# Kernel optimization log

Hardware: AMD Instinct MI355X
Metric: run time of the kernel (lower is better)

## Reference

```python
import jax, jax.numpy as jnp
import numpy as np

N_NODES = 100000
N_EDGES = 640000
D_IN = 128
D_OUT = 128


def setup_inputs() -> dict:
    key = jax.random.key(0)
    k_x, k_w, k_v, k_r, k_c = jax.random.split(key, 5)
    x = jax.random.normal(k_x, (N_NODES, D_IN), dtype=jnp.float32)
    # Xavier-uniform init for weights, zeros for bias (matches module init)
    limit = float(np.sqrt(6.0 / (D_IN + D_OUT)))
    weights = jax.random.uniform(k_w, (D_IN, D_OUT), dtype=jnp.float32,
                                 minval=-limit, maxval=limit)
    bias = jnp.zeros((D_OUT,), dtype=jnp.float32)
    # Sparse normalized adjacency in COO form: value[e] * y[col[e]] scattered to row[e]
    edge_val = jax.random.uniform(k_v, (N_EDGES,), dtype=jnp.float32)
    row = jax.random.randint(k_r, (N_EDGES,), 0, N_NODES, dtype=jnp.int32)
    col = jax.random.randint(k_c, (N_EDGES,), 0, N_NODES, dtype=jnp.int32)
    return {"x": x, "weights": weights, "bias": bias,
            "edge_val": edge_val, "row": row, "col": col}


def reference(x, weights, bias, edge_val, row, col):
    # y = x @ W  (dense GEMM)  [N, D_OUT]
    y = x @ weights
    # SpMM: out[i] = sum_{e: row[e]==i} edge_val[e] * y[col[e]]
    msg = edge_val[:, None] * y[col]            # [E, D_OUT] irregular gather
    agg = jax.ops.segment_sum(msg, row, num_segments=x.shape[0])
    return agg + bias
```

## Files before the change

### kernel.cpp

```cpp
#include <hip/hip_runtime.h>
#include <hip/hip_bf16.h>


#define N_NODES 100000
#define N_EDGES 640000
#define D 128
#define ELL_K 16
#define OVF_CAP 8192
#define NB 391
#define BCAP 2048
#define CHUNK 4096
#define NCHUNKS 157
#define N_TILES 6250
#define YT_P 132

typedef __attribute__((ext_vector_type(8))) short short8;
typedef __attribute__((ext_vector_type(4))) float f32x4;
typedef __attribute__((ext_vector_type(4))) ushort us4;

__device__ __forceinline__ ushort f2bf(float f) {
    __hip_bfloat16 h = __float2bfloat16(f);
    return __builtin_bit_cast(ushort, h);
}
__device__ __forceinline__ float bflo(uint u) { return __uint_as_float(u << 16); }
__device__ __forceinline__ float bfhi(uint u) { return __uint_as_float(u & 0xffff0000u); }

__global__ __launch_bounds__(256, 2) void gemm_xw(const float* __restrict__ x,
                                                  const float* __restrict__ w,
                                                  ushort* __restrict__ y,
                                                  int* __restrict__ bucketCnt) {
    __shared__ ushort wt[128 * 128];
    __shared__ ushort ytile[4][16 * YT_P];
    const int tid = threadIdx.x;

    int gz = blockIdx.x * 256 + tid;
    if (gz <= NB) bucketCnt[gz] = 0;

    #pragma unroll
    for (int it = 0; it < 16; ++it) {
        int idx4 = tid + it * 256;
        int k = idx4 >> 5;
        int n0 = (idx4 & 31) * 4;
        float4 v = *(const float4*)(w + (size_t)idx4 * 4);
        float vv[4] = {v.x, v.y, v.z, v.w};
        #pragma unroll
        for (int q = 0; q < 4; ++q) {
            int n = n0 + q;
            wt[n * 128 + (k ^ ((n & 7) << 3))] = f2bf(vv[q]);
        }
    }
    __syncthreads();

    const int lane = tid & 63;
    const int l15 = lane & 15;
    const int h = lane >> 4;
    const int wv = tid >> 6;
    ushort* yt = &ytile[wv][0];

    short8 bfr[8][4];
    #pragma unroll
    for (int j = 0; j < 8; ++j) {
        int n = 16 * j + l15;
        #pragma unroll
        for (int ks = 0; ks < 4; ++ks) {
            int k0 = 32 * ks + 8 * h;
            bfr[j][ks] = *(const short8*)&wt[n * 128 + (k0 ^ ((n & 7) << 3))];
        }
    }

    const int waveGlobal = blockIdx.x * 4 + wv;
    const int nWaves = gridDim.x * 4;

    int t = waveGlobal;
    if (t < N_TILES) {
        short8 a[4];
        {
            const float* xr = x + (size_t)(t * 16 + l15) * D;
            float4 xb[8];
            #pragma unroll
            for (int ks = 0; ks < 4; ++ks) {
                xb[2 * ks]     = *(const float4*)(xr + 32 * ks + 8 * h);
                xb[2 * ks + 1] = *(const float4*)(xr + 32 * ks + 8 * h + 4);
            }
            #pragma unroll
            for (int ks = 0; ks < 4; ++ks) {
                const float* p0 = (const float*)&xb[2 * ks];
                const float* p1 = (const float*)&xb[2 * ks + 1];
                a[ks][0] = f2bf(p0[0]); a[ks][1] = f2bf(p0[1]);
                a[ks][2] = f2bf(p0[2]); a[ks][3] = f2bf(p0[3]);
                a[ks][4] = f2bf(p1[0]); a[ks][5] = f2bf(p1[1]);
                a[ks][6] = f2bf(p1[2]); a[ks][7] = f2bf(p1[3]);
            }
        }
        #pragma unroll 1
        while (true) {
            const int tn = t + nWaves;
            const bool more = tn < N_TILES;

            float4 xb2[8];
            if (more) {
                const float* xr = x + (size_t)(tn * 16 + l15) * D;
                #pragma unroll
                for (int ks = 0; ks < 4; ++ks) {
                    xb2[2 * ks]     = *(const float4*)(xr + 32 * ks + 8 * h);
                    xb2[2 * ks + 1] = *(const float4*)(xr + 32 * ks + 8 * h + 4);
                }
            }

            f32x4 acc[8];
            #pragma unroll
            for (int j = 0; j < 8; ++j) acc[j] = (f32x4){0.f, 0.f, 0.f, 0.f};
            #pragma unroll
            for (int ks = 0; ks < 4; ++ks) {
                #pragma unroll
                for (int j = 0; j < 8; ++j)
                    acc[j] = __builtin_amdgcn_mfma_f32_16x16x32_bf16(bfr[j][ks], a[ks], acc[j], 0, 0, 0);
            }

            #pragma unroll
            for (int j = 0; j < 8; ++j) {
                us4 o;
                o.x = f2bf(acc[j][0]); o.y = f2bf(acc[j][1]);
                o.z = f2bf(acc[j][2]); o.w = f2bf(acc[j][3]);
                *(us4*)(yt + l15 * YT_P + 16 * j + 4 * h) = o;
            }
            ushort* yn = y + (size_t)(t * 16) * D;
            #pragma unroll
            for (int q = 0; q < 4; ++q) {
                int nl = 4 * q + h;
                float4 v = *(const float4*)(yt + nl * YT_P + l15 * 8);
                *(float4*)(yn + (size_t)nl * D + l15 * 8) = v;
            }

            if (!more) break;
            #pragma unroll
            for (int ks = 0; ks < 4; ++ks) {
                const float* p0 = (const float*)&xb2[2 * ks];
                const float* p1 = (const float*)&xb2[2 * ks + 1];
                a[ks][0] = f2bf(p0[0]); a[ks][1] = f2bf(p0[1]);
                a[ks][2] = f2bf(p0[2]); a[ks][3] = f2bf(p0[3]);
                a[ks][4] = f2bf(p1[0]); a[ks][5] = f2bf(p1[1]);
                a[ks][6] = f2bf(p1[2]); a[ks][7] = f2bf(p1[3]);
            }
            t = tn;
        }
    }
}

__global__ __launch_bounds__(256) void partition_edges(const float* __restrict__ ev,
                                                       const int* __restrict__ row,
                                                       const int* __restrict__ col,
                                                       int* __restrict__ bucketCnt,
                                                       uint2* __restrict__ es0,
                                                       int* __restrict__ ovfCnt,
                                                       int* __restrict__ ovfRow,
                                                       int* __restrict__ ovfCol,
                                                       float* __restrict__ ovfVal) {
    __shared__ int hist[NB];
    __shared__ int cur[NB];
    const int tid = threadIdx.x;
    const int base = blockIdx.x * CHUNK;

    for (int t = tid; t < NB; t += 256) hist[t] = 0;
    __syncthreads();

    #pragma unroll
    for (int it = 0; it < CHUNK / 256; ++it) {
        int i = base + it * 256 + tid;
        if (i < N_EDGES) atomicAdd(&hist[row[i] >> 8], 1);
    }
    __syncthreads();

    for (int t = tid; t < NB; t += 256) {
        int h = hist[t];
        int start = (h > 0) ? atomicAdd(&bucketCnt[t], h) : 0;
        cur[t] = t * BCAP + start;
    }
    __syncthreads();

    #pragma unroll
    for (int it = 0; it < CHUNK / 256; ++it) {
        int i = base + it * 256 + tid;
        if (i < N_EDGES) {
            int r = row[i];
            int b = r >> 8;
            int p = atomicAdd(&cur[b], 1);
            if (p < (b + 1) * BCAP) {
                uint2 e;
                e.x = __float_as_uint(ev[i]);
                e.y = (uint)col[i] | ((uint)(r & 255) << 20);
                es0[p] = e;
            } else {
                int q = atomicAdd(ovfCnt, 1);
                if (q < OVF_CAP) {
                    ovfRow[q] = r;
                    ovfCol[q] = col[i];
                    ovfVal[q] = ev[i];
                }
            }
        }
    }
}

__global__ __launch_bounds__(256) void build_ell(const uint2* __restrict__ es0,
                                                 const int* __restrict__ bucketCnt,
                                                 float2* __restrict__ es,
                                                 int* __restrict__ counts,
                                                 int* __restrict__ ovfCnt,
                                                 int* __restrict__ ovfRow,
                                                 int* __restrict__ ovfCol,
                                                 float* __restrict__ ovfVal) {
    __shared__ float2 ell[256 * ELL_K];
    __shared__ int lcnt[256];
    const int tid = threadIdx.x;
    const int b = blockIdx.x;

    lcnt[tid] = 0;
    __syncthreads();

    int cnt = bucketCnt[b];
    if (cnt > BCAP) cnt = BCAP;
    const uint2* src = es0 + (size_t)b * BCAP;

    for (int i = tid; i < cnt; i += 256) {
        uint2 e = src[i];
        int r = e.y >> 20;
        int p = atomicAdd(&lcnt[r], 1);
        if (p < ELL_K) {
            float2 rec;
            rec.x = __uint_as_float(e.x);
            rec.y = __uint_as_float(e.y & 0xFFFFFu);
            ell[r * ELL_K + p] = rec;
        } else {
            int q = atomicAdd(ovfCnt, 1);
            if (q < OVF_CAP) {
                ovfRow[q] = b * 256 + r;
                ovfCol[q] = (int)(e.y & 0xFFFFFu);
                ovfVal[q] = __uint_as_float(e.x);
            }
        }
    }
    __syncthreads();

    const int nbase = b * 256;
    int nvalid = N_NODES - nbase;
    if (nvalid > 256) nvalid = 256;

    if (tid < nvalid) counts[nbase + tid] = lcnt[tid];

    float4* dst4 = (float4*)(es + (size_t)nbase * ELL_K);
    const float4* ell4 = (const float4*)ell;
    for (int t = tid; t < nvalid * (ELL_K / 2); t += 256)
        dst4[t] = ell4[t];
}

__global__ __launch_bounds__(256) void spmm_ell(const ushort* __restrict__ y,
                                                const float2* __restrict__ es,
                                                const int* __restrict__ counts,
                                                const float* __restrict__ bias,
                                                float* __restrict__ out) {
    const int tid = threadIdx.x;
    const int lane = tid & 63;
    const int c16 = lane & 15;
    const int sub = lane >> 4;
    const int wid = blockIdx.x * 4 + (tid >> 6);

    const float4 b0 = *(const float4*)(bias + c16 * 8);
    const float4 b1 = *(const float4*)(bias + c16 * 8 + 4);

    #pragma unroll 1
    for (int rep = 0; rep < 2; ++rep) {
        const int n = wid * 8 + rep * 4 + sub;
        int deg = counts[n];
        if (deg > ELL_K) deg = ELL_K;
        const float4* er = (const float4*)(es + (size_t)n * ELL_K);

        float a0 = 0.f, a1 = 0.f, a2 = 0.f, a3 = 0.f;
        float a4 = 0.f, a5 = 0.f, a6 = 0.f, a7 = 0.f;

        #pragma unroll
        for (int g = 0; g < 4; ++g) {
            if (4 * g < deg) {
                float4 sA = er[2 * g];
                float4 sB = er[2 * g + 1];
                int c0 = __float_as_int(sA.y);
                int c1 = (4 * g + 1 < deg) ? __float_as_int(sA.w) : c0;
                int c2 = (4 * g + 2 < deg) ? __float_as_int(sB.y) : c0;
                int c3 = (4 * g + 3 < deg) ? __float_as_int(sB.w) : c0;
                uint4 u0 = *(const uint4*)(y + ((size_t)c0 << 7) + c16 * 8);
                uint4 u1 = *(const uint4*)(y + ((size_t)c1 << 7) + c16 * 8);
                uint4 u2 = *(const uint4*)(y + ((size_t)c2 << 7) + c16 * 8);
                uint4 u3 = *(const uint4*)(y + ((size_t)c3 << 7) + c16 * 8);
                float v0 = sA.x;
                float v1 = (4 * g + 1 < deg) ? sA.z : 0.f;
                float v2 = (4 * g + 2 < deg) ? sB.x : 0.f;
                float v3 = (4 * g + 3 < deg) ? sB.z : 0.f;
                a0 += v0 * bflo(u0.x); a1 += v0 * bfhi(u0.x);
                a2 += v0 * bflo(u0.y); a3 += v0 * bfhi(u0.y);
                a4 += v0 * bflo(u0.z); a5 += v0 * bfhi(u0.z);
                a6 += v0 * bflo(u0.w); a7 += v0 * bfhi(u0.w);
                a0 += v1 * bflo(u1.x); a1 += v1 * bfhi(u1.x);
                a2 += v1 * bflo(u1.y); a3 += v1 * bfhi(u1.y);
                a4 += v1 * bflo(u1.z); a5 += v1 * bfhi(u1.z);
                a6 += v1 * bflo(u1.w); a7 += v1 * bfhi(u1.w);
                a0 += v2 * bflo(u2.x); a1 += v2 * bfhi(u2.x);
                a2 += v2 * bflo(u2.y); a3 += v2 * bfhi(u2.y);
                a4 += v2 * bflo(u2.z); a5 += v2 * bfhi(u2.z);
                a6 += v2 * bflo(u2.w); a7 += v2 * bfhi(u2.w);
                a0 += v3 * bflo(u3.x); a1 += v3 * bfhi(u3.x);
                a2 += v3 * bflo(u3.y); a3 += v3 * bfhi(u3.y);
                a4 += v3 * bflo(u3.z); a5 += v3 * bfhi(u3.z);
                a6 += v3 * bflo(u3.w); a7 += v3 * bfhi(u3.w);
            }
        }
        float4 o0 = {a0 + b0.x, a1 + b0.y, a2 + b0.z, a3 + b0.w};
        float4 o1 = {a4 + b1.x, a5 + b1.y, a6 + b1.z, a7 + b1.w};
        float* orow = out + ((size_t)n << 7) + c16 * 8;
        *(float4*)orow = o0;
        *(float4*)(orow + 4) = o1;
    }
}

__global__ void ovf_fix(const ushort* __restrict__ y, const int* __restrict__ ovfRow,
                        const int* __restrict__ ovfCol, const float* __restrict__ ovfVal,
                        const int* __restrict__ ovfCnt, float* __restrict__ out) {
    int nOvf = *ovfCnt;
    if (nOvf > OVF_CAP) nOvf = OVF_CAP;
    int total = nOvf * 32;
    for (int idx = blockIdx.x * 256 + threadIdx.x; idx < total; idx += gridDim.x * 256) {
        int e = idx >> 5;
        int c = idx & 31;
        int r = ovfRow[e];
        int col = ovfCol[e];
        float v = ovfVal[e];
        uint2 u = *(const uint2*)(y + ((size_t)col << 7) + c * 4);
        atomicAdd(&out[(size_t)r * D + c * 4 + 0], v * bflo(u.x));
        atomicAdd(&out[(size_t)r * D + c * 4 + 1], v * bfhi(u.x));
        atomicAdd(&out[(size_t)r * D + c * 4 + 2], v * bflo(u.y));
        atomicAdd(&out[(size_t)r * D + c * 4 + 3], v * bfhi(u.y));
    }
}

extern "C" void kernel_launch(void* const* d_in, const int* in_sizes, int n_in,
                              void* d_out, int out_size, void* d_ws, size_t ws_size,
                              hipStream_t stream) {
    const float* x = (const float*)d_in[0];
    const float* w = (const float*)d_in[1];
    const float* bias = (const float*)d_in[2];
    const float* ev = (const float*)d_in[3];
    const int* row = (const int*)d_in[4];
    const int* col = (const int*)d_in[5];
    float* out = (float*)d_out;

    size_t off = 0;
    auto carve = [&](size_t bytes) -> void* {
        void* p = (char*)d_ws + off;
        off += (bytes + 255) & ~(size_t)255;
        return p;
    };
    ushort* y = (ushort*)carve((size_t)N_NODES * D * sizeof(ushort));
    int* counts = (int*)carve((size_t)N_NODES * sizeof(int));
    float2* es = (float2*)carve((size_t)N_NODES * ELL_K * sizeof(float2));
    uint2* es0 = (uint2*)carve((size_t)NB * BCAP * sizeof(uint2));
    int* bucketCnt = (int*)carve((NB + 1) * sizeof(int));
    int* ovfCnt = bucketCnt + NB;
    int* ovfRow = (int*)carve(OVF_CAP * sizeof(int));
    int* ovfCol = (int*)carve(OVF_CAP * sizeof(int));
    float* ovfVal = (float*)carve(OVF_CAP * sizeof(float));

    gemm_xw<<<512, 256, 0, stream>>>(x, w, y, bucketCnt);
    partition_edges<<<NCHUNKS, 256, 0, stream>>>(ev, row, col, bucketCnt, es0,
                                                 ovfCnt, ovfRow, ovfCol, ovfVal);
    build_ell<<<NB, 256, 0, stream>>>(es0, bucketCnt, es, counts,
                                      ovfCnt, ovfRow, ovfCol, ovfVal);
    spmm_ell<<<N_NODES / 32, 256, 0, stream>>>(y, es, counts, bias, out);
    ovf_fix<<<16, 256, 0, stream>>>(y, ovfRow, ovfCol, ovfVal, ovfCnt, out);
}
```

Measured before the change: 83.70 us.

## Fuse edge partitioning into GEMM kernel with atomic dynamic tile scheduling

Merges the edge-partition kernel into the GEMM kernel. The first NCHUNKS blocks bucket edges before they join the GEMM, and all waves pull 16-row tiles from a global atomic ticket counter instead of a static stride, so blocks that did partition work simply take fewer tiles. This removes one kernel launch and lets partitioning overlap with the GEMM, but adds a memset launch and a global atomic per tile. The cross-iteration x prefetch is also reduced: the next tile's load now happens after the y store rather than before the MFMAs.

```diff
diff --git a/kernel.cpp b/kernel.cpp
--- a/kernel.cpp
+++ b/kernel.cpp
@@ -13,6 +13,7 @@
 #define NCHUNKS 157
 #define N_TILES 6250
 #define YT_P 132
+#define GRID 512
 
 typedef __attribute__((ext_vector_type(8))) short short8;
 typedef __attribute__((ext_vector_type(4))) float f32x4;
@@ -25,16 +26,66 @@
 __device__ __forceinline__ float bflo(uint u) { return __uint_as_float(u << 16); }
 __device__ __forceinline__ float bfhi(uint u) { return __uint_as_float(u & 0xffff0000u); }
 
-__global__ __launch_bounds__(256, 2) void gemm_xw(const float* __restrict__ x,
-                                                  const float* __restrict__ w,
-                                                  ushort* __restrict__ y,
-                                                  int* __restrict__ bucketCnt) {
-    __shared__ ushort wt[128 * 128];
-    __shared__ ushort ytile[4][16 * YT_P];
+__global__ __launch_bounds__(256, 2) void gemm_part(const float* __restrict__ x,
+                                                    const float* __restrict__ w,
+                                                    ushort* __restrict__ y,
+                                                    const float* __restrict__ ev,
+                                                    const int* __restrict__ row,
+                                                    const int* __restrict__ col,
+                                                    uint2* __restrict__ es0,
+                                                    int* __restrict__ ctrl,
+                                                    int* __restrict__ ovfRow,
+                                                    int* __restrict__ ovfCol,
+                                                    float* __restrict__ ovfVal) {
+    __shared__ union {
+        struct { ushort wt[128 * 128]; ushort ytile[4][16 * YT_P]; } g;
+        struct { int hist[NB]; int cur[NB]; } p;
+    } sm;
     const int tid = threadIdx.x;
-
-    int gz = blockIdx.x * 256 + tid;
-    if (gz <= NB) bucketCnt[gz] = 0;
+    int* tick = ctrl + 0;
+    int* ovfCnt = ctrl + 1;
+    int* bucketCnt = ctrl + 2;
+
+    if (blockIdx.x < NCHUNKS) {
+        const int base = blockIdx.x * CHUNK;
+        for (int t = tid; t < NB; t += 256) sm.p.hist[t] = 0;
+        __syncthreads();
+        #pragma unroll
+        for (int it = 0; it < CHUNK / 256; ++it) {
+            int i = base + it * 256 + tid;
+            if (i < N_EDGES) atomicAdd(&sm.p.hist[row[i] >> 8], 1);
+        }
+        __syncthreads();
+        for (int t = tid; t < NB; t += 256) {
+            int h = sm.p.hist[t];
+            int start = (h > 0) ? atomicAdd(&bucketCnt[t], h) : 0;
+            sm.p.cur[t] = t * BCAP + start;
+        }
+        __syncthreads();
+        #pragma unroll
+        for (int it = 0; it < CHUNK / 256; ++it) {
+            int i = base + it * 256 + tid;
+            if (i < N_EDGES) {
+                int r = row[i];
+                int b = r >> 8;
+                int p = atomicAdd(&sm.p.cur[b], 1);
+                if (p < (b + 1) * BCAP) {
+                    uint2 e;
+                    e.x = __float_as_uint(ev[i]);
+                    e.y = (uint)col[i] | ((uint)(r & 255) << 20);
+                    es0[p] = e;
+                } else {
+                    int q = atomicAdd(ovfCnt, 1);
+                    if (q < OVF_CAP) {
+                        ovfRow[q] = r;
+                        ovfCol[q] = col[i];
+                        ovfVal[q] = ev[i];
+                    }
+                }
+            }
+        }
+        __syncthreads();
+    }
 
     #pragma unroll
     for (int it = 0; it < 16; ++it) {
@@ -46,7 +97,7 @@
         #pragma unroll
         for (int q = 0; q < 4; ++q) {
             int n = n0 + q;
-            wt[n * 128 + (k ^ ((n & 7) << 3))] = f2bf(vv[q]);
+            sm.g.wt[n * 128 + (k ^ ((n & 7) << 3))] = f2bf(vv[q]);
         }
     }
     __syncthreads();
@@ -55,7 +106,7 @@
     const int l15 = lane & 15;
     const int h = lane >> 4;
     const int wv = tid >> 6;
-    ushort* yt = &ytile[wv][0];
+    ushort* yt = &sm.g.ytile[wv][0];
 
     short8 bfr[8][4];
     #pragma unroll
@@ -64,17 +115,16 @@
         #pragma unroll
         for (int ks = 0; ks < 4; ++ks) {
             int k0 = 32 * ks + 8 * h;
-            bfr[j][ks] = *(const short8*)&wt[n * 128 + (k0 ^ ((n & 7) << 3))];
-        }
-    }
-
-    const int waveGlobal = blockIdx.x * 4 + wv;
-    const int nWaves = gridDim.x * 4;
-
-    int t = waveGlobal;
-    if (t < N_TILES) {
-        short8 a[4];
-        {
+            bfr[j][ks] = *(const short8*)&sm.g.wt[n * 128 + (k0 ^ ((n & 7) << 3))];
+        }
+    }
+
+    short8 a[4];
+    int t;
+    {
+        if (lane == 0) t = atomicAdd(tick, 1);
+        t = __shfl(t, 0);
+        if (t < N_TILES) {
             const float* xr = x + (size_t)(t * 16 + l15) * D;
             float4 xb[8];
             #pragma unroll
@@ -92,113 +142,56 @@
                 a[ks][6] = f2bf(p1[2]); a[ks][7] = f2bf(p1[3]);
             }
         }
-        #pragma unroll 1
-        while (true) {
-            const int tn = t + nWaves;
-            const bool more = tn < N_TILES;
-
-            float4 xb2[8];
-            if (more) {
-                const float* xr = x + (size_t)(tn * 16 + l15) * D;
-                #pragma unroll
-                for (int ks = 0; ks < 4; ++ks) {
-                    xb2[2 * ks]     = *(const float4*)(xr + 32 * ks + 8 * h);
-                    xb2[2 * ks + 1] = *(const float4*)(xr + 32 * ks + 8 * h + 4);
-                }
-            }
-
-            f32x4 acc[8];
-            #pragma unroll
-            for (int j = 0; j < 8; ++j) acc[j] = (f32x4){0.f, 0.f, 0.f, 0.f};
+    }
+    #pragma unroll 1
+    while (t < N_TILES) {
+        int tn_;
+        if (lane == 0) tn_ = atomicAdd(tick, 1);
+
+        f32x4 acc[8];
+        #pragma unroll
+        for (int j = 0; j < 8; ++j) acc[j] = (f32x4){0.f, 0.f, 0.f, 0.f};
+        #pragma unroll
+        for (int ks = 0; ks < 4; ++ks) {
+            #pragma unroll
+            for (int j = 0; j < 8; ++j)
+                acc[j] = __builtin_amdgcn_mfma_f32_16x16x32_bf16(bfr[j][ks], a[ks], acc[j], 0, 0, 0);
+        }
+        #pragma unroll
+        for (int j = 0; j < 8; ++j) {
+            us4 o;
+            o.x = f2bf(acc[j][0]); o.y = f2bf(acc[j][1]);
+            o.z = f2bf(acc[j][2]); o.w = f2bf(acc[j][3]);
+            *(us4*)(yt + l15 * YT_P + 16 * j + 4 * h) = o;
+        }
+        ushort* yn = y + (size_t)(t * 16) * D;
+        #pragma unroll
+        for (int q = 0; q < 4; ++q) {
+            int nl = 4 * q + h;
+            float4 v = *(const float4*)(yt + nl * YT_P + l15 * 8);
+            *(float4*)(yn + (size_t)nl * D + l15 * 8) = v;
+        }
+
+        int tn = __shfl(tn_, 0);
+        if (tn < N_TILES) {
+            const float* xr = x + (size_t)(tn * 16 + l15) * D;
+            float4 xb[8];
             #pragma unroll
             for (int ks = 0; ks < 4; ++ks) {
-                #pragma unroll
-                for (int j = 0; j < 8; ++j)
-                    acc[j] = __builtin_amdgcn_mfma_f32_16x16x32_bf16(bfr[j][ks], a[ks], acc[j], 0, 0, 0);
-            }
-
-            #pragma unroll
-            for (int j = 0; j < 8; ++j) {
-                us4 o;
-                o.x = f2bf(acc[j][0]); o.y = f2bf(acc[j][1]);
-                o.z = f2bf(acc[j][2]); o.w = f2bf(acc[j][3]);
-                *(us4*)(yt + l15 * YT_P + 16 * j + 4 * h) = o;
-            }
-            ushort* yn = y + (size_t)(t * 16) * D;
-            #pragma unroll
-            for (int q = 0; q < 4; ++q) {
-                int nl = 4 * q + h;
-                float4 v = *(const float4*)(yt + nl * YT_P + l15 * 8);
-                *(float4*)(yn + (size_t)nl * D + l15 * 8) = v;
-            }
-
-            if (!more) break;
+                xb[2 * ks]     = *(const float4*)(xr + 32 * ks + 8 * h);
+                xb[2 * ks + 1] = *(const float4*)(xr + 32 * ks + 8 * h + 4);
+            }
             #pragma unroll
             for (int ks = 0; ks < 4; ++ks) {
-                const float* p0 = (const float*)&xb2[2 * ks];
-                const float* p1 = (const float*)&xb2[2 * ks + 1];
+                const float* p0 = (const float*)&xb[2 * ks];
+                const float* p1 = (const float*)&xb[2 * ks + 1];
                 a[ks][0] = f2bf(p0[0]); a[ks][1] = f2bf(p0[1]);
                 a[ks][2] = f2bf(p0[2]); a[ks][3] = f2bf(p0[3]);
                 a[ks][4] = f2bf(p1[0]); a[ks][5] = f2bf(p1[1]);
                 a[ks][6] = f2bf(p1[2]); a[ks][7] = f2bf(p1[3]);
             }
-            t = tn;
-        }
-    }
-}
-
-__global__ __launch_bounds__(256) void partition_edges(const float* __restrict__ ev,
-                                                       const int* __restrict__ row,
-                                                       const int* __restrict__ col,
-                                                       int* __restrict__ bucketCnt,
-                                                       uint2* __restrict__ es0,
-                                                       int* __restrict__ ovfCnt,
-                                                       int* __restrict__ ovfRow,
-                                                       int* __restrict__ ovfCol,
-                                                       float* __restrict__ ovfVal) {
-    __shared__ int hist[NB];
-    __shared__ int cur[NB];
-    const int tid = threadIdx.x;
-    const int base = blockIdx.x * CHUNK;
-
-    for (int t = tid; t < NB; t += 256) hist[t] = 0;
-    __syncthreads();
-
-    #pragma unroll
-    for (int it = 0; it < CHUNK / 256; ++it) {
-        int i = base + it * 256 + tid;
-        if (i < N_EDGES) atomicAdd(&hist[row[i] >> 8], 1);
-    }
-    __syncthreads();
-
-    for (int t = tid; t < NB; t += 256) {
-        int h = hist[t];
-        int start = (h > 0) ? atomicAdd(&bucketCnt[t], h) : 0;
-        cur[t] = t * BCAP + start;
-    }
-    __syncthreads();
-
-    #pragma unroll
-    for (int it = 0; it < CHUNK / 256; ++it) {
-        int i = base + it * 256 + tid;
-        if (i < N_EDGES) {
-            int r = row[i];
-            int b = r >> 8;
-            int p = atomicAdd(&cur[b], 1);
-            if (p < (b + 1) * BCAP) {
-                uint2 e;
-                e.x = __float_as_uint(ev[i]);
-                e.y = (uint)col[i] | ((uint)(r & 255) << 20);
-                es0[p] = e;
-            } else {
-                int q = atomicAdd(ovfCnt, 1);
-                if (q < OVF_CAP) {
-                    ovfRow[q] = r;
-                    ovfCol[q] = col[i];
-                    ovfVal[q] = ev[i];
-                }
-            }
-        }
+        }
+        t = tn;
     }
 }
 
@@ -362,15 +355,16 @@
     int* counts = (int*)carve((size_t)N_NODES * sizeof(int));
     float2* es = (float2*)carve((size_t)N_NODES * ELL_K * sizeof(float2));
     uint2* es0 = (uint2*)carve((size_t)NB * BCAP * sizeof(uint2));
-    int* bucketCnt = (int*)carve((NB + 1) * sizeof(int));
-    int* ovfCnt = bucketCnt + NB;
+    int* ctrl = (int*)carve((2 + NB) * sizeof(int));
+    int* ovfCnt = ctrl + 1;
+    int* bucketCnt = ctrl + 2;
     int* ovfRow = (int*)carve(OVF_CAP * sizeof(int));
     int* ovfCol = (int*)carve(OVF_CAP * sizeof(int));
     float* ovfVal = (float*)carve(OVF_CAP * sizeof(float));
 
-    gemm_xw<<<512, 256, 0, stream>>>(x, w, y, bucketCnt);
-    partition_edges<<<NCHUNKS, 256, 0, stream>>>(ev, row, col, bucketCnt, es0,
-                                                 ovfCnt, ovfRow, ovfCol, ovfVal);
+    hipMemsetAsync(ctrl, 0, (2 + NB) * sizeof(int), stream);
+    gemm_part<<<GRID, 256, 0, stream>>>(x, w, y, ev, row, col, es0, ctrl,
+                                        ovfRow, ovfCol, ovfVal);
     build_ell<<<NB, 256, 0, stream>>>(es0, bucketCnt, es, counts,
                                       ovfCnt, ovfRow, ovfCol, ovfVal);
     spmm_ell<<<N_NODES / 32, 256, 0, stream>>>(y, es, counts, bias, out);
```

Result: slower. 167.2 us (+99.7%).
